# Performance work log

Measured on AMD Instinct MI355X. Metric: run time of the kernel, lower is better.

## Reference

```python
import jax, jax.numpy as jnp
import numpy as np
from jax import lax

B, S, D, F, E, K = 4, 2048, 2048, 8192, 8, 2


def setup_inputs() -> dict:
    key = jax.random.key(0)
    ks = jax.random.split(key, 4)
    sd = 1.0 / np.sqrt(D)
    sf = 1.0 / np.sqrt(F)
    return {
        "hidden_states": jax.random.normal(ks[0], (B, S, D), dtype=jnp.float32),
        "router_w": jax.random.normal(ks[1], (D, E), dtype=jnp.float32) * sd,
        "w1": jax.random.normal(ks[2], (E, D, F), dtype=jnp.float32) * sd,
        "b1": jnp.zeros((E, F), dtype=jnp.float32),
        "w2": jax.random.normal(ks[3], (E, F, D), dtype=jnp.float32) * sf,
        "b2": jnp.zeros((E, D), dtype=jnp.float32),
        "top_k": K,
    }


def reference(hidden_states, router_w, w1, b1, w2, b2, top_k):
    b, s, d = hidden_states.shape
    x = hidden_states.reshape(-1, d)  # [T, D] flat tokens
    # Router: top-k over expert logits, softmax over the selected logits.
    logits = x @ router_w                      # [T, E]
    top_vals, top_idx = lax.top_k(logits, top_k)  # [T, K]
    scores = jax.nn.softmax(top_vals, axis=-1)    # [T, K]

    out = jnp.zeros_like(x)
    n_experts = w1.shape[0]
    for e in range(n_experts):  # fixed small expert count
        # per-token combine weight for this expert (0 if not routed)
        cw = jnp.sum(jnp.where(top_idx == e, scores, 0.0), axis=-1)  # [T]
        h = jax.nn.gelu(x @ w1[e] + b1[e], approximate=False)        # [T, F]
        out = out + cw[:, None] * (h @ w2[e] + b2[e])                # masked combine
    out = out.reshape(b, s, d)
    return out + hidden_states  # use_residual=True
```

## Files before the change

### kernel.cpp

```cpp
#include <hip/hip_runtime.h>

#define T_TOK 8192
#define DIM   2048
#define FFN   8192
#define NE    8
#define TOPK  2

typedef unsigned short ushort_t;
typedef unsigned short ushort8  __attribute__((ext_vector_type(8)));
typedef unsigned short ushort4v __attribute__((ext_vector_type(4)));
typedef short bf16x8 __attribute__((ext_vector_type(8)));
typedef float f32x4  __attribute__((ext_vector_type(4)));

__device__ __forceinline__ ushort_t f2bf(float f) {
  unsigned int u = __float_as_uint(f);
  u += 0x7FFFu + ((u >> 16) & 1u);
  return (ushort_t)(u >> 16);
}
__device__ __forceinline__ float bf2f(ushort_t u) {
  return __uint_as_float(((unsigned int)u) << 16);
}

__device__ __forceinline__ void gload16(const void* g, void* l) {
  __builtin_amdgcn_global_load_lds((const __attribute__((address_space(1))) void*)g,
                                   (__attribute__((address_space(3))) void*)l, 16, 0, 0);
}
__device__ __forceinline__ unsigned lds_off(const ushort_t* p) {
  return (unsigned)(uintptr_t)(__attribute__((address_space(3))) const ushort_t*)p;
}
__device__ __forceinline__ bf16x8 ds_read128(unsigned off) {
  bf16x8 r;
  asm volatile("ds_read_b128 %0, %1" : "=v"(r) : "v"(off));
  return r;
}

__device__ __forceinline__ float gelu_exact(float v) {
  float s = v * 0.70710678118654752f;
  float a = fabsf(s);
  float t = __builtin_amdgcn_rcpf(1.0f + 0.3275911f * a);
  float p = t * (0.254829592f +
            t * (-0.284496736f +
            t * (1.421413741f +
            t * (-1.453152027f +
            t * 1.061405429f))));
  float er = 1.0f - p * __expf(-a * a);
  er = copysignf(er, s);
  return 0.5f * v * (1.0f + er);
}

__global__ __launch_bounds__(256) void k_router(
    const float* __restrict__ x, const float* __restrict__ rw, ushort_t* __restrict__ xbf,
    int* __restrict__ tidx, float* __restrict__ twt, int* __restrict__ counts) {
  int t = blockIdx.x;
  int tid = threadIdx.x;
  int lane = tid & 63, wave = tid >> 6;
  float acc[NE];
#pragma unroll
  for (int e = 0; e < NE; e++) acc[e] = 0.f;
  const float* xr = x + (size_t)t * DIM;
  ushort_t* xbr = xbf + (size_t)t * DIM;
#pragma unroll
  for (int it = 0; it < 2; it++) {
    int d4 = it * 1024 + tid * 4;
    float4 v = *reinterpret_cast<const float4*>(xr + d4);
    ushort4v o;
    o.x = f2bf(v.x); o.y = f2bf(v.y); o.z = f2bf(v.z); o.w = f2bf(v.w);
    *reinterpret_cast<ushort4v*>(xbr + d4) = o;
    const float* r0p = rw + (size_t)d4 * NE;
    float xv[4] = {v.x, v.y, v.z, v.w};
#pragma unroll
    for (int j = 0; j < 4; j++) {
      const float* r = r0p + j * NE;
#pragma unroll
      for (int e = 0; e < NE; e++) acc[e] += xv[j] * r[e];
    }
  }
  __shared__ float wsum[4][NE];
#pragma unroll
  for (int e = 0; e < NE; e++) {
    float v = acc[e];
#pragma unroll
    for (int off = 32; off > 0; off >>= 1) v += __shfl_down(v, off);
    if (lane == 0) wsum[wave][e] = v;
  }
  __syncthreads();
  if (tid == 0) {
    float lg[NE];
#pragma unroll
    for (int e = 0; e < NE; e++) lg[e] = wsum[0][e] + wsum[1][e] + wsum[2][e] + wsum[3][e];
    int i0 = 0; float v0 = lg[0];
#pragma unroll
    for (int e = 1; e < NE; e++) if (lg[e] > v0) { v0 = lg[e]; i0 = e; }
    int i1 = -1; float v1 = -3.4e38f;
#pragma unroll
    for (int e = 0; e < NE; e++) if (e != i0 && lg[e] > v1) { v1 = lg[e]; i1 = e; }
    float e1 = expf(v1 - v0);
    float s = 1.f + e1;
    tidx[t * 2 + 0] = i0; tidx[t * 2 + 1] = i1;
    twt[t * 2 + 0] = 1.f / s; twt[t * 2 + 1] = e1 / s;
    atomicAdd(&counts[i0], 1);
    atomicAdd(&counts[i1], 1);
  }
}

#define TT 64
__global__ __launch_bounds__(256) void k_wcvt(const float* __restrict__ in,
                                              ushort_t* __restrict__ outp, int R, int C) {
  __shared__ float t[TT][TT + 1];
  int e = blockIdx.z;
  const float* src = in + (size_t)e * R * C;
  ushort_t* dst = outp + (size_t)e * R * C;
  int r0 = blockIdx.y * TT, c0 = blockIdx.x * TT;
  int tid = threadIdx.x;
  int rr = tid >> 4;
  int c4 = tid & 15;
#pragma unroll
  for (int i = 0; i < 4; i++) {
    int r = rr + i * 16;
    float4 v = *reinterpret_cast<const float4*>(src + (size_t)(r0 + r) * C + c0 + c4 * 4);
    t[r][c4 * 4 + 0] = v.x; t[r][c4 * 4 + 1] = v.y;
    t[r][c4 * 4 + 2] = v.z; t[r][c4 * 4 + 3] = v.w;
  }
  __syncthreads();
  int c = tid >> 2, rs = tid & 3;
  ushort8 v0, v1;
#pragma unroll
  for (int i = 0; i < 8; i++) {
    v0[i] = f2bf(t[rs * 16 + i][c]);
    v1[i] = f2bf(t[rs * 16 + 8 + i][c]);
  }
  ushort_t* drow = dst + (size_t)(c0 + c) * R + r0 + rs * 16;
  *reinterpret_cast<ushort8*>(drow) = v0;
  *reinterpret_cast<ushort8*>(drow + 8) = v1;
}

__global__ void k_scan(const int* __restrict__ counts, int* __restrict__ offsets) {
  if (threadIdx.x == 0) {
    int s = 0;
    for (int e = 0; e < NE; e++) { offsets[e] = s; s += counts[e]; }
    offsets[NE] = s;
  }
}

__global__ void k_fill(const int* __restrict__ tidx, const float* __restrict__ twt,
                       const int* __restrict__ offsets, int* __restrict__ cursors,
                       int* __restrict__ ltok, float* __restrict__ lwt, int* __restrict__ ppos) {
  int t = blockIdx.x * blockDim.x + threadIdx.x;
  if (t >= T_TOK) return;
#pragma unroll
  for (int k = 0; k < TOPK; k++) {
    int e = tidx[t * 2 + k];
    int pos = atomicAdd(&cursors[e], 1);
    int p = offsets[e] + pos;
    ltok[p] = t;
    lwt[p] = twt[t * 2 + k];
    ppos[t * 2 + k] = p;
  }
}

__device__ __forceinline__ void xcd_decode(int lin, int nwg, int nx, int& xt, int& yt) {
  int q = nwg >> 3;
  int w = (lin & 7) * q + (lin >> 3);
  xt = w % nx;
  yt = w / nx;
}

#define QBM 256
#define QBN 256
#define QBK 64
#define QHALF_E (128 * 64)
#define QSLOT_E (2 * QHALF_E)

#define RD_A(RR, qq)                                                                    \
  RR[0][0] = ds_read128(aoff[(qq) * 2 + 0][0] + cb);                                    \
  RR[0][1] = ds_read128(aoff[(qq) * 2 + 0][1] + cb);                                    \
  RR[1][0] = ds_read128(aoff[(qq) * 2 + 1][0] + cb);                                    \
  RR[1][1] = ds_read128(aoff[(qq) * 2 + 1][1] + cb);

#define PH_MFMA(qq, RR)                                                                 \
  __builtin_amdgcn_s_setprio(1);                                                        \
  _Pragma("unroll")                                                                     \
  for (int mf = 0; mf < 2; mf++)                                                        \
    _Pragma("unroll")                                                                   \
    for (int nf = 0; nf < 4; nf++) {                                                    \
      acc[(qq) * 2 + mf][nf] = __builtin_amdgcn_mfma_f32_16x16x32_bf16(                 \
          RR[mf][0], bv[nf][0], acc[(qq) * 2 + mf][nf], 0, 0, 0);                       \
      acc[(qq) * 2 + mf][nf] = __builtin_amdgcn_mfma_f32_16x16x32_bf16(                 \
          RR[mf][1], bv[nf][1], acc[(qq) * 2 + mf][nf], 0, 0, 0);                       \
    }                                                                                   \
  __builtin_amdgcn_s_setprio(0);

#define GEMM8_PIPE(NT_)                                                                 \
  const int NT = (NT_);                                                                 \
  STA(0, 0, 0); STA(0, 1, 0);                                                           \
  STB(0, 0, 0); STB(0, 1, 0);                                                           \
  STB(1, 0, QBK); STB(1, 1, QBK);                                                       \
  asm volatile("s_waitcnt vmcnt(4)" ::: "memory");                                      \
  for (int T = 0; T < NT; ++T) {                                                        \
    int slot = T & 1;                                                                   \
    unsigned cb = (unsigned)(slot * QSLOT_E * 2);                                       \
    bf16x8 bv[4][2], rA[2][2], rB[2][2];                                                \
                                                                                \
    __builtin_amdgcn_sched_barrier(0);                                                  \
    __builtin_amdgcn_s_barrier();                                                       \
    __builtin_amdgcn_sched_barrier(0);                                                  \
    _Pragma("unroll")                                                                   \
    for (int n = 0; n < 4; n++) {                                                       \
      bv[n][0] = ds_read128(boff[n][0] + cb);                                           \
      bv[n][1] = ds_read128(boff[n][1] + cb);                                           \
    }                                                                                   \
    RD_A(rA, 0)                                                                         \
    RD_A(rB, 1)                                                                         \
    if (T + 1 < NT) { STA(slot ^ 1, 0, (T + 1) * QBK); }                                \
    __builtin_amdgcn_sched_barrier(0);                                                  \
    asm volatile("s_waitcnt lgkmcnt(4)" ::: "memory");                                  \
    __builtin_amdgcn_sched_barrier(0);                                                  \
    PH_MFMA(0, rA)                                                                      \
                                                                                \
    __builtin_amdgcn_sched_barrier(0);                                                  \
    __builtin_amdgcn_s_barrier();                                                       \
    __builtin_amdgcn_sched_barrier(0);                                                  \
    RD_A(rA, 2)                                                                         \
    if (T + 1 < NT) { STA(slot ^ 1, 1, (T + 1) * QBK); }                                \
    if (T + 2 < NT) { STB(slot, 0, (T + 2) * QBK); }                                    \
    __builtin_amdgcn_sched_barrier(0);                                                  \
    asm volatile("s_waitcnt lgkmcnt(4)" ::: "memory");                                  \
    __builtin_amdgcn_sched_barrier(0);                                                  \
    PH_MFMA(1, rB)                                                                      \
                               \
    __builtin_amdgcn_sched_barrier(0);                                                  \
    RD_A(rB, 3)                                                                         \
    if (T + 2 < NT) { STB(slot, 1, (T + 2) * QBK); }                                    \
    __builtin_amdgcn_sched_barrier(0);                                                  \
    asm volatile("s_waitcnt lgkmcnt(4)" ::: "memory");                                  \
    __builtin_amdgcn_sched_barrier(0);                                                  \
    PH_MFMA(2, rA)                                                                      \
                                                               \
    __builtin_amdgcn_sched_barrier(0);                                                  \
    asm volatile("s_waitcnt lgkmcnt(0)" ::: "memory");                                  \
    __builtin_amdgcn_sched_barrier(0);                                                  \
    PH_MFMA(3, rB)                                                                      \
    __builtin_amdgcn_sched_barrier(0);                                                  \
    if (T < NT - 2) { asm volatile("s_waitcnt vmcnt(4)" ::: "memory"); }                \
    else            { asm volatile("s_waitcnt vmcnt(0)" ::: "memory"); }                \
    __builtin_amdgcn_sched_barrier(0);                                                  \
  }

#define GEMM8_SETUP()                                                                   \
  int tid = threadIdx.x;                                                                \
  int wid = tid >> 6, lane = tid & 63;                                                  \
  int wm = wid >> 2, wn = wid & 3;                                                      \
  int lm = lane & 15, lg = lane >> 4;                                                   \
  unsigned abase = lds_off(As), bbase = lds_off(Bs);                                    \
  unsigned aoff[8][2], boff[4][2];                                                      \
  _Pragma("unroll")                                                                     \
  for (int m = 0; m < 8; m++)                                                           \
    _Pragma("unroll")                                                                   \
    for (int kk = 0; kk < 2; kk++)                                                      \
      aoff[m][kk] = abase + (unsigned)((wm * QHALF_E + (m * 16 + lm) * 64 +             \
                                        (((kk * 4 + lg) ^ (lm & 7)) * 8)) * 2);         \
  _Pragma("unroll")                                                                     \
  for (int n = 0; n < 4; n++)                                                           \
    _Pragma("unroll")                                                                   \
    for (int kk = 0; kk < 2; kk++)                                                      \
      boff[n][kk] = bbase + (unsigned)(((wn >> 1) * QHALF_E +                           \
                                        ((wn & 1) * 64 + n * 16 + lm) * 64 +            \
                                        (((kk * 4 + lg) ^ (lm & 7)) * 8)) * 2);         \
  f32x4 acc[8][4];                                                                      \
  _Pragma("unroll")                                                                     \
  for (int m = 0; m < 8; m++)                                                           \
    _Pragma("unroll")                                                                   \
    for (int n = 0; n < 4; n++) acc[m][n] = (f32x4){0.f, 0.f, 0.f, 0.f};

__global__ __launch_bounds__(512) void k_gemm1(
    const ushort_t* __restrict__ xbf, const ushort_t* __restrict__ w1t, const float* __restrict__ b1,
    const int* __restrict__ counts, const int* __restrict__ offsets,
    const int* __restrict__ ltok, ushort_t* __restrict__ H) {
  int e = blockIdx.z;
  int cnt = counts[e];
  int xt, yt;
  xcd_decode(blockIdx.x, (T_TOK / QBM) * (FFN / QBN), T_TOK / QBM, xt, yt);
  int row0 = xt * QBM;
  if (row0 >= cnt) return;
  int base = offsets[e];
  int col0 = yt * QBN;
  const ushort_t* Bt = w1t + (size_t)e * DIM * FFN;

  __shared__ __align__(16) ushort_t As[2 * QSLOT_E];
  __shared__ __align__(16) ushort_t Bs[2 * QSLOT_E];

  const ushort_t* aS[2][2]; const ushort_t* bS[2][2];
#pragma unroll
  for (int l = 0; l < 2; l++) {
    int c = l * 512 + threadIdx.x;
    int rr = c >> 3;
    int s8 = (c & 7) ^ (rr & 7);
#pragma unroll
    for (int h = 0; h < 2; h++) {
      int ar = min(row0 + h * 128 + rr, cnt - 1);
      aS[h][l] = xbf + (size_t)ltok[base + ar] * DIM + s8 * 8;
      bS[h][l] = Bt + (size_t)(col0 + h * 128 + rr) * DIM + s8 * 8;
    }
  }
  int swid = threadIdx.x >> 6;
  auto STA = [&](int slot, int h, int k0) {
#pragma unroll
    for (int l = 0; l < 2; l++)
      gload16(aS[h][l] + k0, As + slot * QSLOT_E + h * QHALF_E + (l * 512 + swid * 64) * 8);
  };
  auto STB = [&](int slot, int h, int k0) {
#pragma unroll
    for (int l = 0; l < 2; l++)
      gload16(bS[h][l] + k0, Bs + slot * QSLOT_E + h * QHALF_E + (l * 512 + swid * 64) * 8);
  };

  GEMM8_SETUP();
  GEMM8_PIPE(DIM / QBK);

#pragma unroll
  for (int m = 0; m < 8; m++) {
#pragma unroll
    for (int n = 0; n < 4; n++) {
      int f = col0 + wn * 64 + n * 16 + lm;
      float bias = b1[e * FFN + f];
#pragma unroll
      for (int r = 0; r < 4; r++) {
        int row = row0 + wm * 128 + m * 16 + lg * 4 + r;
        if (row < cnt) {
          float v = acc[m][n][r] + bias;
          H[(size_t)(base + row) * FFN + f] = f2bf(gelu_exact(v));
        }
      }
    }
  }
}

__global__ __launch_bounds__(512) void k_gemm2(
    const ushort_t* __restrict__ H, const ushort_t* __restrict__ w2t, const float* __restrict__ b2,
    const int* __restrict__ counts, const int* __restrict__ offsets,
    const float* __restrict__ lwt, ushort_t* __restrict__ contrib) {
  int e = blockIdx.z;
  int cnt = counts[e];
  int xt, yt;
  xcd_decode(blockIdx.x, (T_TOK / QBM) * (DIM / QBN), T_TOK / QBM, xt, yt);
  int row0 = xt * QBM;
  if (row0 >= cnt) return;
  int base = offsets[e];
  int col0 = yt * QBN;
  const ushort_t* Bt = w2t + (size_t)e * DIM * FFN;

  __shared__ __align__(16) ushort_t As[2 * QSLOT_E];
  __shared__ __align__(16) ushort_t Bs[2 * QSLOT_E];

  const ushort_t* aS[2][2]; const ushort_t* bS[2][2];
#pragma unroll
  for (int l = 0; l < 2; l++) {
    int c = l * 512 + threadIdx.x;
    int rr = c >> 3;
    int s8 = (c & 7) ^ (rr & 7);
#pragma unroll
    for (int h = 0; h < 2; h++) {
      int ar = min(row0 + h * 128 + rr, cnt - 1);
      aS[h][l] = H + (size_t)(base + ar) * FFN + s8 * 8;
      bS[h][l] = Bt + (size_t)(col0 + h * 128 + rr) * FFN + s8 * 8;
    }
  }
  int swid = threadIdx.x >> 6;
  auto STA = [&](int slot, int h, int k0) {
#pragma unroll
    for (int l = 0; l < 2; l++)
      gload16(aS[h][l] + k0, As + slot * QSLOT_E + h * QHALF_E + (l * 512 + swid * 64) * 8);
  };
  auto STB = [&](int slot, int h, int k0) {
#pragma unroll
    for (int l = 0; l < 2; l++)
      gload16(bS[h][l] + k0, Bs + slot * QSLOT_E + h * QHALF_E + (l * 512 + swid * 64) * 8);
  };

  GEMM8_SETUP();
  GEMM8_PIPE(FFN / QBK);

#pragma unroll
  for (int m = 0; m < 8; m++) {
#pragma unroll
    for (int n = 0; n < 4; n++) {
      int d = col0 + wn * 64 + n * 16 + lm;
      float bias = b2[e * DIM + d];
#pragma unroll
      for (int r = 0; r < 4; r++) {
        int row = row0 + wm * 128 + m * 16 + lg * 4 + r;
        if (row < cnt) {
          float v = (acc[m][n][r] + bias) * lwt[base + row];
          contrib[(size_t)(base + row) * DIM + d] = f2bf(v);
        }
      }
    }
  }
}

__global__ void k_combine(const float* __restrict__ x, const ushort_t* __restrict__ contrib,
                          const int* __restrict__ ppos, float* __restrict__ out) {
  int i = blockIdx.x * blockDim.x + threadIdx.x;
  int t = i / (DIM / 4);
  int dq = i % (DIM / 4);
  int p0 = ppos[t * 2 + 0], p1 = ppos[t * 2 + 1];
  float4 xv = reinterpret_cast<const float4*>(x)[i];
  ushort4v c0 = reinterpret_cast<const ushort4v*>(contrib + (size_t)p0 * DIM)[dq];
  ushort4v c1 = reinterpret_cast<const ushort4v*>(contrib + (size_t)p1 * DIM)[dq];
  float4 o;
  o.x = xv.x + bf2f(c0.x) + bf2f(c1.x);
  o.y = xv.y + bf2f(c0.y) + bf2f(c1.y);
  o.z = xv.z + bf2f(c0.z) + bf2f(c1.z);
  o.w = xv.w + bf2f(c0.w) + bf2f(c1.w);
  reinterpret_cast<float4*>(out)[i] = o;
}

extern "C" void kernel_launch(void* const* d_in, const int* in_sizes, int n_in,
                              void* d_out, int out_size, void* d_ws, size_t ws_size,
                              hipStream_t stream) {
  const float* x  = (const float*)d_in[0];
  const float* rw = (const float*)d_in[1];
  const float* w1 = (const float*)d_in[2];
  const float* b1 = (const float*)d_in[3];
  const float* w2 = (const float*)d_in[4];
  const float* b2 = (const float*)d_in[5];
  float* out = (float*)d_out;
  char* ws = (char*)d_ws;

  const size_t MB = 1u << 20;
  int*   counts  = (int*)(ws);
  int*   offsets = (int*)(ws + 64);
  int*   cursors = (int*)(ws + 128);
  int*   tidx    = (int*)(ws + 1 * MB);
  float* twt     = (float*)(ws + 2 * MB);
  int*   ltok    = (int*)(ws + 3 * MB);
  float* lwt     = (float*)(ws + 4 * MB);
  int*   ppos    = (int*)(ws + 5 * MB);
  ushort_t* xbf     = (ushort_t*)(ws + 8 * MB);
  ushort_t* contrib = (ushort_t*)(ws + 8 * MB);
  ushort_t* Hbuf    = (ushort_t*)(ws + 72 * MB);
  ushort_t* w1t     = (ushort_t*)(ws + 328 * MB);
  ushort_t* w2t     = (ushort_t*)(ws + 328 * MB);
  const size_t NEED = 584 * MB;
  if (ws_size < NEED) {
    hipMemsetAsync(d_out, 0, (size_t)out_size * sizeof(float), stream);
    return;
  }

  hipMemsetAsync(ws, 0, 256, stream);
  k_router<<<T_TOK, 256, 0, stream>>>(x, rw, xbf, tidx, twt, counts);
  k_scan<<<1, 64, 0, stream>>>(counts, offsets);
  k_fill<<<T_TOK / 256, 256, 0, stream>>>(tidx, twt, offsets, cursors, ltok, lwt, ppos);
  k_wcvt<<<dim3(FFN / TT, DIM / TT, NE), 256, 0, stream>>>(w1, w1t, DIM, FFN);
  k_gemm1<<<dim3((T_TOK / QBM) * (FFN / QBN), 1, NE), 512, 0, stream>>>(xbf, w1t, b1, counts, offsets, ltok, Hbuf);
  k_wcvt<<<dim3(DIM / TT, FFN / TT, NE), 256, 0, stream>>>(w2, w2t, FFN, DIM);
  k_gemm2<<<dim3((T_TOK / QBM) * (DIM / QBN), 1, NE), 512, 0, stream>>>(Hbuf, w2t, b2, counts, offsets, lwt, contrib);
  k_combine<<<dim3((T_TOK * (size_t)DIM / 4) / 256), 256, 0, stream>>>(x, contrib, ppos, out);
}
```

Before: 1.892 ms.

## Triple-buffer A tiles in LDS to prefetch two K-steps ahead

Expands the A operand LDS buffer from two to three slots, using rotating read and write indices, so A tiles are loaded two iterations ahead to match the existing B prefetch depth. The prologue now issues two stages of both A and B loads. The aim is to hide the latency of gathered global loads of A rows better. In exchange LDS use per block grows (A goes from 64KB to 96KB, for 160KB total), and the vmcnt wait counts were not changed, so the waits may be wrong for the new number of loads in flight.

```diff
diff --git a/kernel.cpp b/kernel.cpp
--- a/kernel.cpp
+++ b/kernel.cpp
@@ -171,11 +171,11 @@
 #define QHALF_E (128 * 64)
 #define QSLOT_E (2 * QHALF_E)
 
-#define RD_A(RR, qq)                                                                    \
-  RR[0][0] = ds_read128(aoff[(qq) * 2 + 0][0] + cb);                                    \
-  RR[0][1] = ds_read128(aoff[(qq) * 2 + 0][1] + cb);                                    \
-  RR[1][0] = ds_read128(aoff[(qq) * 2 + 1][0] + cb);                                    \
-  RR[1][1] = ds_read128(aoff[(qq) * 2 + 1][1] + cb);
+#define RD_A(RR, qq, CB)                                                                \
+  RR[0][0] = ds_read128(aoff[(qq) * 2 + 0][0] + (CB));                                  \
+  RR[0][1] = ds_read128(aoff[(qq) * 2 + 0][1] + (CB));                                  \
+  RR[1][0] = ds_read128(aoff[(qq) * 2 + 1][0] + (CB));                                  \
+  RR[1][1] = ds_read128(aoff[(qq) * 2 + 1][1] + (CB));
 
 #define PH_MFMA(qq, RR)                                                                 \
   __builtin_amdgcn_s_setprio(1);                                                        \
@@ -192,13 +192,13 @@
 
 #define GEMM8_PIPE(NT_)                                                                 \
   const int NT = (NT_);                                                                 \
-  STA(0, 0, 0); STA(0, 1, 0);                                                           \
-  STB(0, 0, 0); STB(0, 1, 0);                                                           \
-  STB(1, 0, QBK); STB(1, 1, QBK);                                                       \
+  STA(0, 0, 0); STB(0, 0, 0); STA(0, 1, 0); STB(0, 1, 0);                               \
+  STA(1, 0, QBK); STB(1, 0, QBK); STA(1, 1, QBK); STB(1, 1, QBK);                       \
   asm volatile("s_waitcnt vmcnt(4)" ::: "memory");                                      \
+  int ard = 0, awr = 2;                                                                 \
   for (int T = 0; T < NT; ++T) {                                                        \
-    int slot = T & 1;                                                                   \
-    unsigned cb = (unsigned)(slot * QSLOT_E * 2);                                       \
+    unsigned cbA = (unsigned)(ard * QSLOT_E * 2);                                       \
+    unsigned cbB = (unsigned)((T & 1) * QSLOT_E * 2);                                   \
     bf16x8 bv[4][2], rA[2][2], rB[2][2];                                                \
                                                                                 \
     __builtin_amdgcn_sched_barrier(0);                                                  \
@@ -206,12 +206,12 @@
     __builtin_amdgcn_sched_barrier(0);                                                  \
     _Pragma("unroll")                                                                   \
     for (int n = 0; n < 4; n++) {                                                       \
-      bv[n][0] = ds_read128(boff[n][0] + cb);                                           \
-      bv[n][1] = ds_read128(boff[n][1] + cb);                                           \
+      bv[n][0] = ds_read128(boff[n][0] + cbB);                                          \
+      bv[n][1] = ds_read128(boff[n][1] + cbB);                                          \
     }                                                                                   \
-    RD_A(rA, 0)                                                                         \
-    RD_A(rB, 1)                                                                         \
-    if (T + 1 < NT) { STA(slot ^ 1, 0, (T + 1) * QBK); }                                \
+    RD_A(rA, 0, cbA)                                                                    \
+    RD_A(rB, 1, cbA)                                                                    \
+    if (T + 2 < NT) { STA(awr, 0, (T + 2) * QBK); }                                     \
     __builtin_amdgcn_sched_barrier(0);                                                  \
     asm volatile("s_waitcnt lgkmcnt(4)" ::: "memory");                                  \
     __builtin_amdgcn_sched_barrier(0);                                                  \
@@ -220,17 +220,17 @@
     __builtin_amdgcn_sched_barrier(0);                                                  \
     __builtin_amdgcn_s_barrier();                                                       \
     __builtin_amdgcn_sched_barrier(0);                                                  \
-    RD_A(rA, 2)                                                                         \
-    if (T + 1 < NT) { STA(slot ^ 1, 1, (T + 1) * QBK); }                                \
-    if (T + 2 < NT) { STB(slot, 0, (T + 2) * QBK); }                                    \
+    RD_A(rA, 2, cbA)                                                                    \
+    if (T + 2 < NT) { STA(awr, 1, (T + 2) * QBK); }                                     \
+    if (T + 2 < NT) { STB(T & 1, 0, (T + 2) * QBK); }                                   \
     __builtin_amdgcn_sched_barrier(0);                                                  \
     asm volatile("s_waitcnt lgkmcnt(4)" ::: "memory");                                  \
     __builtin_amdgcn_sched_barrier(0);                                                  \
     PH_MFMA(1, rB)                                                                      \
-                               \
-    __builtin_amdgcn_sched_barrier(0);                                                  \
-    RD_A(rB, 3)                                                                         \
-    if (T + 2 < NT) { STB(slot, 1, (T + 2) * QBK); }                                    \
+                                      \
+    __builtin_amdgcn_sched_barrier(0);                                                  \
+    RD_A(rB, 3, cbA)                                                                    \
+    if (T + 2 < NT) { STB(T & 1, 1, (T + 2) * QBK); }                                   \
     __builtin_amdgcn_sched_barrier(0);                                                  \
     asm volatile("s_waitcnt lgkmcnt(4)" ::: "memory");                                  \
     __builtin_amdgcn_sched_barrier(0);                                                  \
@@ -244,6 +244,8 @@
     if (T < NT - 2) { asm volatile("s_waitcnt vmcnt(4)" ::: "memory"); }                \
     else            { asm volatile("s_waitcnt vmcnt(0)" ::: "memory"); }                \
     __builtin_amdgcn_sched_barrier(0);                                                  \
+    ard = (ard + 1 == 3) ? 0 : ard + 1;                                                 \
+    awr = (awr + 1 == 3) ? 0 : awr + 1;                                                 \
   }
 
 #define GEMM8_SETUP()                                                                   \
@@ -286,7 +288,7 @@
   int col0 = yt * QBN;
   const ushort_t* Bt = w1t + (size_t)e * DIM * FFN;
 
-  __shared__ __align__(16) ushort_t As[2 * QSLOT_E];
+  __shared__ __align__(16) ushort_t As[3 * QSLOT_E];
   __shared__ __align__(16) ushort_t Bs[2 * QSLOT_E];
 
   const ushort_t* aS[2][2]; const ushort_t* bS[2][2];
@@ -349,7 +351,7 @@
   int col0 = yt * QBN;
   const ushort_t* Bt = w2t + (size_t)e * DIM * FFN;
 
-  __shared__ __align__(16) ushort_t As[2 * QSLOT_E];
+  __shared__ __align__(16) ushort_t As[3 * QSLOT_E];
   __shared__ __align__(16) ushort_t Bs[2 * QSLOT_E];
 
   const ushort_t* aS[2][2]; const ushort_t* bS[2][2];
```

New measurement: 1.949 ms. 1.03x slower.
